# Performance work log

Hardware: AMD Instinct MI355X
Metric: run time of the kernel (lower is better)

Reference implementation:

```python
import jax, jax.numpy as jnp
import numpy as np

NH = 4       # n_heads
R = 3        # n_rounds
LN_EPS = 1e-5
NEG = -1e9   # large negative for masked attention (avoids NaN on fully-masked rows)


def _mha(q, k, v, w, b, block=None):
    # w: [4, D, D] = (Wq, Wk, Wv, Wo); b: [4, D]. batch_first MHA, no dropout (eval).
    B, Nq, Dm = q.shape
    hd = Dm // NH

    def proj(x, wi, bi):
        return (x @ wi + bi).reshape(B, -1, NH, hd).transpose(0, 2, 1, 3)  # [B,h,N,hd]

    Q = proj(q, w[0], b[0])
    K = proj(k, w[1], b[1])
    V = proj(v, w[2], b[2])
    s = jnp.einsum('bhqd,bhkd->bhqk', Q, K) * (1.0 / np.sqrt(hd))
    if block is not None:  # block[b,q,k]=True means masked out
        s = jnp.where(block[:, None, :, :], NEG, s)
    p = jax.nn.softmax(s, axis=-1)
    o = jnp.einsum('bhqk,bhkd->bhqd', p, V).transpose(0, 2, 1, 3).reshape(B, -1, Dm)
    return o @ w[3] + b[3]


def setup_inputs() -> dict:
    key = jax.random.key(0)
    ks = jax.random.split(key, 16)
    B, N, Dm = 256, 128, 256
    s = 0.02
    return {
        'H': jax.random.normal(ks[0], (B, N, Dm), jnp.float32),
        'pred_heads': jax.random.randint(ks[1], (B, N), 0, N),
        'mask': jnp.ones((B, N), jnp.float32),
        'ha_w': jax.random.normal(ks[2], (R, 4, Dm, Dm)) * s,
        'ha_b': jnp.zeros((R, 4, Dm)),
        'sa_w': jax.random.normal(ks[3], (R, 4, Dm, Dm)) * s,
        'sa_b': jnp.zeros((R, 4, Dm)),
        'ct_w': jax.random.normal(ks[4], (R, 2 * Dm, Dm)) * s,
        'ct_b': jnp.zeros((R, Dm)),
        'gate_w': jax.random.normal(ks[5], (R, 4 * Dm, Dm)) * s,
        'gate_b': jnp.zeros((R, Dm)),
        'tr_w': jax.random.normal(ks[6], (R, 4 * Dm, Dm)) * s,
        'tr_b': jnp.zeros((R, Dm)),
        'ln_g': jnp.ones((R, Dm)),
        'ln_b': jnp.zeros((R, Dm)),
        'arc_head_w': jax.random.normal(ks[7], (Dm, Dm)) * s,
        'arc_head_b': jnp.zeros((Dm,)),
        'arc_dep_w': jax.random.normal(ks[8], (Dm, Dm)) * s,
        'arc_dep_b': jnp.zeros((Dm,)),
        'bilinear': jax.random.normal(ks[9], (Dm, Dm)) * np.sqrt(2.0 / Dm).astype(np.float32),
        'bh_w': jax.random.normal(ks[10], (Dm,)) * s,
        'bh_b': jnp.zeros(()),
        'bd_w': jax.random.normal(ks[11], (Dm,)) * s,
        'bd_b': jnp.zeros(()),
    }


def reference(H, pred_heads, mask, ha_w, ha_b, sa_w, sa_b, ct_w, ct_b,
              gate_w, gate_b, tr_w, tr_b, ln_g, ln_b,
              arc_head_w, arc_head_b, arc_dep_w, arc_dep_b, bilinear,
              bh_w, bh_b, bd_w, bd_b):
    B, N, Dm = H.shape
    mb = mask > 0
    hi = jnp.clip(pred_heads, 0, N - 1)
    hi3 = jnp.broadcast_to(hi[:, :, None], (B, N, Dm))
    bidx = jnp.arange(B)[:, None]
    eye = jnp.eye(N, dtype=bool)
    # sibling mask: same predicted head, not self, both positions valid (constant across rounds)
    sib = (pred_heads[:, :, None] == pred_heads[:, None, :]) & ~eye[None] \
          & mb[:, None, :] & mb[:, :, None]
    block = ~sib

    Hr = H
    for i in range(R):
        # gather head representation, attend to it
        head_repr = jnp.take_along_axis(Hr, hi3, axis=1)
        head_msg = _mha(Hr, head_repr, head_repr, ha_w[i], ha_b[i])
        # scatter-add children onto their heads, average
        child_sum = jnp.zeros_like(Hr).at[bidx, hi].add(Hr)
        child_count = jnp.zeros((B, N), Hr.dtype).at[bidx, hi].add(mask)
        child_avg = child_sum / jnp.maximum(child_count, 1.0)[:, :, None]
        child_msg = jax.nn.gelu(
            jnp.concatenate([Hr, child_avg], -1) @ ct_w[i] + ct_b[i], approximate=False)
        # masked sibling self-attention (N <= 128 branch)
        sib_msg = _mha(Hr, Hr, Hr, sa_w[i], sa_b[i], block=block)
        # gated fuse + residual + LayerNorm
        comb = jnp.concatenate([Hr, head_msg, child_msg, sib_msg], -1)
        g = jax.nn.sigmoid(comb @ gate_w[i] + gate_b[i])
        u = jax.nn.gelu(comb @ tr_w[i] + tr_b[i], approximate=False)
        Hn = Hr + g * u
        mu = Hn.mean(-1, keepdims=True)
        var = ((Hn - mu) ** 2).mean(-1, keepdims=True)
        Hr = (Hn - mu) / jnp.sqrt(var + LN_EPS) * ln_g[i] + ln_b[i]

    h_head = Hr @ arc_head_w + arc_head_b
    h_dep = Hr @ arc_dep_w + arc_dep_b
    scores = jnp.einsum('bnd,de,bme->bnm', h_head, bilinear, h_dep)
    scores = scores + (h_head @ bh_w + bh_b)[:, None, :] + (h_dep @ bd_w + bd_b)[:, :, None]
    return Hr, scores
```

## Files before the change

kernel.cpp:

```cpp
#include <hip/hip_runtime.h>
#include <hip/hip_bf16.h>
#include <math.h>

typedef __hip_bfloat16 bf16;
typedef __attribute__((ext_vector_type(8))) short bf16x8v;
typedef __attribute__((ext_vector_type(4))) float f32x4v;

#define BD 256
#define NN 128
#define DM 256
#define NHD 4
#define HDIM 64
#define RR 3

__device__ __forceinline__ float b2f(bf16 x) { return __bfloat162float(x); }
__device__ __forceinline__ bf16 f2b(float x) { return __float2bfloat16(x); }
__device__ __forceinline__ float geluf(float x) { return 0.5f * x * (1.f + erff(x * 0.70710678118654752f)); }

#define GLOAD16(g, l) __builtin_amdgcn_global_load_lds( \
    (const __attribute__((address_space(1))) void*)(g), \
    (__attribute__((address_space(3))) void*)(l), 16, 0, 0)

__global__ __launch_bounds__(256) void cvt32to16_kernel(
    const float* __restrict__ in, bf16* __restrict__ out, int n)
{
  int i = blockIdx.x * 256 + threadIdx.x;
  int stride = gridDim.x * 256;
  for (; i < n; i += stride) out[i] = f2b(in[i]);
}

__global__ __launch_bounds__(256) void cvt16to32_kernel(
    const bf16* __restrict__ in, float* __restrict__ out, int n)
{
  int i = blockIdx.x * 256 + threadIdx.x;
  int stride = gridDim.x * 256;
  for (; i < n; i += stride) out[i] = b2f(in[i]);
}

struct TDesc { const float* src; bf16* dst; int K; int base; };
struct TTable { TDesc e[11]; };

__global__ __launch_bounds__(256) void transpose_w_kernel(TTable T, int nent)
{
  int t = blockIdx.x;
  int ei = 0;
  for (int i = 1; i < nent; i++) if (t >= T.e[i].base) ei = i;
  const float* src = T.e[ei].src;
  bf16* dst = T.e[ei].dst;
  int K = T.e[ei].K;
  int lt = t - T.e[ei].base;
  int nt = lt & 7, kt = lt >> 3;

  __shared__ float tile[32][33];
  int tx = threadIdx.x & 31, ty = threadIdx.x >> 5;
#pragma unroll
  for (int i = 0; i < 4; i++)
    tile[ty + i * 8][tx] = src[(size_t)(kt * 32 + ty + i * 8) * 256 + nt * 32 + tx];
  __syncthreads();
#pragma unroll
  for (int i = 0; i < 4; i++)
    dst[(size_t)(nt * 32 + ty + i * 8) * K + kt * 32 + tx] = f2b(tile[tx][ty + i * 8]);
}

struct ProjArgs {
  const bf16* Hc; const bf16* CA; const int* gather;
  const bf16* W[7];
  const float* bias[7];
  bf16* out[7];
};

__global__ __launch_bounds__(256) void proj_fused_kernel(ProjArgs P)
{
  const int b  = blockIdx.x & 255;
  const int nh = blockIdx.x >> 8;
  const int c0 = nh * 128;
  const int tid = threadIdx.x;
  const int w = tid >> 6;
  const int lane = tid & 63;
  const int wr = w >> 1, wc = w & 1;
  const int r16 = lane & 15;
  const int kg = lane >> 4;

  __shared__ __align__(16) char lds[81920];

  const char* Hb = (const char*)(P.Hc + (size_t)b * NN * DM);

#pragma unroll
  for (int i = 0; i < 16; i++) {
    int row = w * 32 + i * 2 + (lane >> 5);
    int src = row * 512 + (((lane & 31) * 16) ^ ((row & 7) << 4));
    GLOAD16(Hb + src, lds + w * 16384 + i * 1024);
  }

#define STAGE_W(WT, K2, KT, BUF) do { \
    _Pragma("unroll") \
    for (int i_ = 0; i_ < 2; i_++) { \
      int wrow_ = w * 32 + i_ * 16 + (lane >> 2); \
      int slot_ = (lane & 3) ^ ((wrow_ >> 1) & 3); \
      GLOAD16((const char*)(WT) + (size_t)(c0 + wrow_) * (K2) + (KT) * 64 + slot_ * 16, \
              lds + 65536 + (BUF) * 8192 + w * 2048 + i_ * 1024); \
    } } while (0)

  STAGE_W(P.W[0], 512, 0, 0);
  __syncthreads();

  int lrow[4], grow[4];
#pragma unroll
  for (int mi = 0; mi < 4; mi++) {
    lrow[mi] = wr * 64 + mi * 16 + r16;
    int g = P.gather[b * NN + lrow[mi]];
    grow[mi] = min(max(g, 0), NN - 1);
  }
  int wro[4];
#pragma unroll
  for (int ni = 0; ni < 4; ni++) {
    int ct_ = wc * 64 + ni * 16 + r16;
    wro[ni] = ct_ * 64 + ((kg ^ ((ct_ >> 1) & 3)) << 4);
  }

  const bf16* CAb = P.CA + (size_t)b * NN * DM;
  int buf = 0;
  f32x4v zero = {0.f, 0.f, 0.f, 0.f};

#pragma unroll
  for (int j = 0; j < 7; j++) {
    const bool GATH = (j == 1) || (j == 2);
    const bool TR   = (j == 2) || (j == 5);
    const bool ACT  = (j == 6);
    const int NKS = (j == 6) ? 16 : 8;
    const int K2  = (j == 6) ? 1024 : 512;
    const bf16* Wj  = P.W[j];
    const bf16* Wj1 = (j < 6) ? P.W[j + 1] : P.W[j];
    const int  K2n  = (j < 6) ? ((j + 1 == 6) ? 1024 : 512) : K2;

    f32x4v acc[4][4];
#pragma unroll
    for (int mi = 0; mi < 4; mi++)
#pragma unroll
      for (int ni = 0; ni < 4; ni++) acc[mi][ni] = zero;

    for (int kt = 0; kt < NKS; kt++) {
      if (!(j == 6 && kt + 1 == NKS)) {
        const bf16* Wn = (kt + 1 < NKS) ? Wj : Wj1;
        int nkt = (kt + 1 < NKS) ? kt + 1 : 0;
        int nK2 = (kt + 1 < NKS) ? K2 : K2n;
        STAGE_W(Wn, nK2, nkt, buf ^ 1);
      }

      bf16x8v a[4], wv[4];
      if (j == 6 && kt >= 8) {
#pragma unroll
        for (int mi = 0; mi < 4; mi++)
          a[mi] = *(const bf16x8v*)(CAb + (size_t)lrow[mi] * DM + (kt - 8) * 32 + kg * 8);
      } else {
#pragma unroll
        for (int mi = 0; mi < 4; mi++) {
          int ar = GATH ? grow[mi] : lrow[mi];
          int off = ar * 512 + (((kt * 64) + kg * 16) ^ ((ar & 7) << 4));
          a[mi] = *(const bf16x8v*)(lds + off);
        }
      }
#pragma unroll
      for (int ni = 0; ni < 4; ni++)
        wv[ni] = *(const bf16x8v*)(lds + 65536 + buf * 8192 + wro[ni]);

#pragma unroll
      for (int mi = 0; mi < 4; mi++)
#pragma unroll
        for (int ni = 0; ni < 4; ni++)
          acc[mi][ni] = __builtin_amdgcn_mfma_f32_16x16x32_bf16(a[mi], wv[ni], acc[mi][ni], 0, 0, 0);

      __syncthreads();
      buf ^= 1;
    }

    bf16* outj = P.out[j];
    const float* bj = P.bias[j];
#pragma unroll
    for (int ni = 0; ni < 4; ni++) {
      int col = c0 + wc * 64 + ni * 16 + r16;
      float bv = bj ? bj[col] : 0.f;
#pragma unroll
      for (int mi = 0; mi < 4; mi++) {
        int row0 = wr * 64 + mi * 16 + kg * 4;
        if (!TR) {
          size_t base = ((size_t)b * NN + row0) * DM + col;
#pragma unroll
          for (int r = 0; r < 4; r++) {
            float x = acc[mi][ni][r] + bv;
            if (ACT) x = geluf(x);
            outj[base + (size_t)r * DM] = f2b(x);
          }
        } else {
          size_t base = ((size_t)b * DM + col) * NN + row0;
#pragma unroll
          for (int r = 0; r < 4; r++)
            outj[base + r] = f2b(acc[mi][ni][r] + bv);
        }
      }
    }
  }
#undef STAGE_W
}

struct GJob {
  const bf16 *a0, *a1, *a2, *a3;
  const int* gather;
  const bf16* Wt;
  const float* bias;
  bf16* out;
  int K, act, transp;
};
struct GJobs8 { GJob j[8]; };

__global__ __launch_bounds__(256) void gemm_multi_kernel(GJobs8 J)
{
  const GJob jb = J.j[blockIdx.y];
  const int b  = blockIdx.x & 255;
  const int nh = blockIdx.x >> 8;
  const int tid = threadIdx.x;
  const int w = tid >> 6;
  const int lane = tid & 63;
  const int wr = w >> 1, wc = w & 1;
  const int r16 = lane & 15;
  const int kg = lane >> 4;
  const int K = jb.K;
  const int nk = K >> 5;
  const int c0 = nh * 128;

  __shared__ __align__(16) char lds[32768];

  const int srow = tid >> 2;
  const int skc  = tid & 3;
  const int sl   = skc ^ ((srow >> 1) & 3);
  int g0 = srow, g1 = srow + 64;
  if (jb.gather) {
    int t0 = jb.gather[b * NN + srow];      g0 = min(max(t0, 0), NN - 1);
    int t1 = jb.gather[b * NN + srow + 64]; g1 = min(max(t1, 0), NN - 1);
  }
  const size_t aoff0 = ((size_t)b * NN + g0) * DM + sl * 8;
  const size_t aoff1 = ((size_t)b * NN + g1) * DM + sl * 8;
  const bf16* wsrc0 = jb.Wt + (size_t)(c0 + srow) * K + sl * 8;
  const bf16* wsrc1 = jb.Wt + (size_t)(c0 + srow + 64) * K + sl * 8;
  const int wbase = w * 1024;

  f32x4v zero = {0.f, 0.f, 0.f, 0.f};
  f32x4v acc[4][4];
#pragma unroll
  for (int mi = 0; mi < 4; mi++)
#pragma unroll
    for (int ni = 0; ni < 4; ni++) acc[mi][ni] = zero;

  int a_ro[4], w_ro[4];
#pragma unroll
  for (int mi = 0; mi < 4; mi++) {
    int row = wr * 64 + mi * 16 + r16;
    a_ro[mi] = row * 64 + ((kg ^ ((row >> 1) & 3)) << 4);
  }
#pragma unroll
  for (int ni = 0; ni < 4; ni++) {
    int col = wc * 64 + ni * 16 + r16;
    w_ro[ni] = col * 64 + ((kg ^ ((col >> 1) & 3)) << 4);
  }

  {
    const bf16* Ab = jb.a0;
    GLOAD16(Ab + aoff0, lds + wbase);
    GLOAD16(Ab + aoff1, lds + 4096 + wbase);
    GLOAD16(wsrc0,      lds + 16384 + wbase);
    GLOAD16(wsrc1,      lds + 16384 + 4096 + wbase);
  }
  __syncthreads();

  int cur = 0;
  for (int kt = 0; kt < nk; kt++) {
    if (kt + 1 < nk) {
      int k0 = (kt + 1) << 5;
      int sg = k0 >> 8;
      const bf16* Ab = (sg == 0) ? jb.a0 : ((sg == 1) ? jb.a1 : ((sg == 2) ? jb.a2 : jb.a3));
      int ko = k0 & 255;
      int nb = (cur ^ 1) * 8192;
      GLOAD16(Ab + aoff0 + ko,  lds + nb + wbase);
      GLOAD16(Ab + aoff1 + ko,  lds + nb + 4096 + wbase);
      GLOAD16(wsrc0 + k0,       lds + 16384 + nb + wbase);
      GLOAD16(wsrc1 + k0,       lds + 16384 + nb + 4096 + wbase);
    }

    const char* La = lds + cur * 8192;
    const char* Lw = lds + 16384 + cur * 8192;
    bf16x8v a[4], ww[4];
#pragma unroll
    for (int mi = 0; mi < 4; mi++) a[mi] = *(const bf16x8v*)(La + a_ro[mi]);
#pragma unroll
    for (int ni = 0; ni < 4; ni++) ww[ni] = *(const bf16x8v*)(Lw + w_ro[ni]);
#pragma unroll
    for (int mi = 0; mi < 4; mi++)
#pragma unroll
      for (int ni = 0; ni < 4; ni++)
        acc[mi][ni] = __builtin_amdgcn_mfma_f32_16x16x32_bf16(a[mi], ww[ni], acc[mi][ni], 0, 0, 0);

    __syncthreads();
    cur ^= 1;
  }

#pragma unroll
  for (int ni = 0; ni < 4; ni++) {
    int col = c0 + wc * 64 + ni * 16 + r16;
    float bv = jb.bias ? jb.bias[col] : 0.f;
#pragma unroll
    for (int mi = 0; mi < 4; mi++) {
      int row0 = wr * 64 + mi * 16 + kg * 4;
      if (!jb.transp) {
        size_t base = ((size_t)b * NN + row0) * DM + col;
#pragma unroll
        for (int r = 0; r < 4; r++) {
          float x = acc[mi][ni][r] + bv;
          if (jb.act == 1) x = geluf(x);
          jb.out[base + (size_t)r * DM] = f2b(x);
        }
      } else {
        size_t base = ((size_t)b * DM + col) * NN + row0;
#pragma unroll
        for (int r = 0; r < 4; r++) {
          float x = acc[mi][ni][r] + bv;
          if (jb.act == 1) x = geluf(x);
          jb.out[base + r] = f2b(x);
        }
      }
    }
  }
}

struct AttnArgs {
  const bf16 *Qa, *Ka, *Va; bf16* Oa;
  const bf16 *Qs, *Ks, *Vs; bf16* Os;
};

__global__ __launch_bounds__(256) void attn2_kernel(
    AttnArgs A, const int* __restrict__ ph, const float* __restrict__ mask)
{
  const int b = blockIdx.y, h = blockIdx.x;
  const bool has_mask = (blockIdx.z == 1);
  const bf16* Qb = has_mask ? A.Qs : A.Qa;
  const bf16* Kb = has_mask ? A.Ks : A.Ka;
  const bf16* Vt = has_mask ? A.Vs : A.Va;
  bf16* Ob       = has_mask ? A.Os : A.Oa;

  const int w = threadIdx.x >> 6;
  const int lane = threadIdx.x & 63;
  const int r16 = lane & 15, kg = lane >> 4;
  const int q0 = w * 32;

  __shared__ bf16 P_lds[4][32 * 128];
  __shared__ int   ph_sh[NN];
  __shared__ float mk_sh[NN];

  if (has_mask && threadIdx.x < NN) {
    ph_sh[threadIdx.x] = ph[(size_t)b * NN + threadIdx.x];
    mk_sh[threadIdx.x] = mask[(size_t)b * NN + threadIdx.x];
  }
  __syncthreads();

  const bf16* Qh = Qb + (size_t)b * NN * DM + (size_t)h * HDIM;
  const bf16* Kh = Kb + (size_t)b * NN * DM + (size_t)h * HDIM;
  const bf16* Vh = Vt + ((size_t)b * DM + (size_t)h * HDIM) * NN;

  f32x4v zero = {0.f, 0.f, 0.f, 0.f};

  f32x4v accs[2][8];
#pragma unroll
  for (int mi = 0; mi < 2; mi++)
#pragma unroll
    for (int ni = 0; ni < 8; ni++) accs[mi][ni] = zero;

#pragma unroll
  for (int ks = 0; ks < 2; ks++) {
    int d = ks * 32 + kg * 8;
    bf16x8v a[2], bb[8];
#pragma unroll
    for (int mi = 0; mi < 2; mi++)
      a[mi] = *(const bf16x8v*)(Qh + (size_t)(q0 + mi * 16 + r16) * DM + d);
#pragma unroll
    for (int ni = 0; ni < 8; ni++)
      bb[ni] = *(const bf16x8v*)(Kh + (size_t)(ni * 16 + r16) * DM + d);
#pragma unroll
    for (int mi = 0; mi < 2; mi++)
#pragma unroll
      for (int ni = 0; ni < 8; ni++)
        accs[mi][ni] = __builtin_amdgcn_mfma_f32_16x16x32_bf16(a[mi], bb[ni], accs[mi][ni], 0, 0, 0);
  }

#pragma unroll
  for (int mi = 0; mi < 2; mi++) {
#pragma unroll
    for (int r = 0; r < 4; r++) {
      int wq = mi * 16 + kg * 4 + r;
      int q_e = q0 + wq;
      float v[8];
      float mx = -3.0e38f;
      int qp = 0; float qm = 1.f;
      if (has_mask) { qp = ph_sh[q_e]; qm = mk_sh[q_e]; }
#pragma unroll
      for (int ni = 0; ni < 8; ni++) {
        float s = accs[mi][ni][r] * 0.125f;
        if (has_mask) {
          int t_e = ni * 16 + r16;
          bool sib = (qp == ph_sh[t_e]) && (q_e != t_e) && (qm > 0.f) && (mk_sh[t_e] > 0.f);
          if (!sib) s = -1e9f;
        }
        v[ni] = s;
        mx = fmaxf(mx, s);
      }
#pragma unroll
      for (int o = 1; o < 16; o <<= 1) mx = fmaxf(mx, __shfl_xor(mx, o, 64));
      float sum = 0.f;
#pragma unroll
      for (int ni = 0; ni < 8; ni++) { v[ni] = __expf(v[ni] - mx); sum += v[ni]; }
#pragma unroll
      for (int o = 1; o < 16; o <<= 1) sum += __shfl_xor(sum, o, 64);
      float inv = 1.f / sum;
      int swz = (wq & 7) << 3;
#pragma unroll
      for (int ni = 0; ni < 8; ni++) {
        int t_e = ni * 16 + r16;
        P_lds[w][(wq * 128 + t_e) ^ swz] = f2b(v[ni] * inv);
      }
    }
  }
  __syncthreads();

  f32x4v acco[2][4];
#pragma unroll
  for (int mi = 0; mi < 2; mi++)
#pragma unroll
    for (int ni = 0; ni < 4; ni++) acco[mi][ni] = zero;

#pragma unroll
  for (int kt = 0; kt < 4; kt++) {
    int t = kt * 32 + kg * 8;
    bf16x8v a[2], bb[4];
#pragma unroll
    for (int mi = 0; mi < 2; mi++) {
      int wqr = mi * 16 + r16;
      int idx = (wqr * 128 + t) ^ ((wqr & 7) << 3);
      a[mi] = *(const bf16x8v*)&P_lds[w][idx];
    }
#pragma unroll
    for (int ni = 0; ni < 4; ni++)
      bb[ni] = *(const bf16x8v*)(Vh + (size_t)(ni * 16 + r16) * NN + t);
#pragma unroll
    for (int mi = 0; mi < 2; mi++)
#pragma unroll
      for (int ni = 0; ni < 4; ni++)
        acco[mi][ni] = __builtin_amdgcn_mfma_f32_16x16x32_bf16(a[mi], bb[ni], acco[mi][ni], 0, 0, 0);
  }

#pragma unroll
  for (int ni = 0; ni < 4; ni++) {
    int d = ni * 16 + r16;
#pragma unroll
    for (int mi = 0; mi < 2; mi++) {
      int qrow = q0 + mi * 16 + kg * 4;
      size_t base = ((size_t)b * NN + qrow) * DM + (size_t)h * HDIM + d;
#pragma unroll
      for (int r = 0; r < 4; r++)
        Ob[base + (size_t)r * DM] = f2b(acco[mi][ni][r]);
    }
  }
}

__global__ __launch_bounds__(256) void child_avg2_kernel(
    const bf16* __restrict__ Hr, const int* __restrict__ ph,
    const float* __restrict__ mask, bf16* __restrict__ CA)
{
  const int b = blockIdx.x;
  const int t = threadIdx.x;
  __shared__ int hi[NN];
  __shared__ float mk[NN];
  __shared__ int cnt[NN], off[NN], rnk[NN], lst[NN];
  __shared__ float cntf[NN];

  if (t < NN) {
    int g = ph[(size_t)b * NN + t];
    hi[t] = min(max(g, 0), NN - 1);
    mk[t] = mask[(size_t)b * NN + t];
  }
  __syncthreads();
  if (t < NN) {
    int c = 0, r = 0; float cf = 0.f;
    int me = hi[t];
    for (int j = 0; j < NN; j++) {
      int hj = hi[j];
      c  += (hj == t);
      cf += (hj == t) ? mk[j] : 0.f;
      r  += (j < t) && (hj == me);
    }
    cnt[t] = c; cntf[t] = cf; rnk[t] = r;
  }
  __syncthreads();
  if (t < NN) {
    int o = 0;
    for (int m = 0; m < t; m++) o += cnt[m];
    off[t] = o;
  }
  __syncthreads();
  if (t < NN) lst[off[hi[t]] + rnk[t]] = t;
  __syncthreads();

  const bf16* Hb = Hr + (size_t)b * NN * DM;
  bf16* Cb = CA + (size_t)b * NN * DM;
  const int d = t;
  for (int m = 0; m < NN; m++) {
    float s = 0.f;
    int o = off[m], c = cnt[m];
    for (int i = 0; i < c; i++)
      s += b2f(Hb[(size_t)lst[o + i] * DM + d]);
    Cb[(size_t)m * DM + d] = f2b(s / fmaxf(cntf[m], 1.f));
  }
}

__global__ __launch_bounds__(256) void ln_epi_kernel(
    const bf16* __restrict__ Hr, const bf16* __restrict__ Gp, const bf16* __restrict__ Up,
    const float* __restrict__ lg, const float* __restrict__ lb, bf16* __restrict__ Hout)
{
  const int b = blockIdx.y;
  const int m0 = blockIdx.x * 8;
  const int c = threadIdx.x;
  __shared__ float red[8];
  float lgv = lg[c], lbv = lb[c];
  int wv = c >> 6, ln = c & 63;
  for (int m = 0; m < 8; m++) {
    size_t idx = ((size_t)b * NN + m0 + m) * DM + c;
    float g = 1.f / (1.f + __expf(-b2f(Gp[idx])));
    float u = geluf(b2f(Up[idx]));
    float hn = b2f(Hr[idx]) + g * u;
    float s1 = hn, s2 = hn * hn;
#pragma unroll
    for (int o = 1; o < 64; o <<= 1) { s1 += __shfl_xor(s1, o, 64); s2 += __shfl_xor(s2, o, 64); }
    if (ln == 0) { red[wv] = s1; red[4 + wv] = s2; }
    __syncthreads();
    float sum = red[0] + red[1] + red[2] + red[3];
    float sq  = red[4] + red[5] + red[6] + red[7];
    float mu = sum * (1.f / DM);
    float var = sq * (1.f / DM) - mu * mu;
    float y = (hn - mu) * rsqrtf(var + 1e-5f) * lgv + lbv;
    Hout[idx] = f2b(y);
    __syncthreads();
  }
}

__global__ __launch_bounds__(256) void rhrd_kernel(
    const bf16* __restrict__ hh, const bf16* __restrict__ hd,
    const float* __restrict__ bhw, const float* __restrict__ bhb,
    const float* __restrict__ bdw, const float* __restrict__ bdb,
    float* __restrict__ rh, float* __restrict__ rd)
{
  int b = blockIdx.x;
  int t = threadIdx.x;
  int n = t & 127;
  bool isD = t >= 128;
  const bf16* row = (isD ? hd : hh) + ((size_t)b * NN + n) * DM;
  const float* wv = isD ? bdw : bhw;
  float s = isD ? bdb[0] : bhb[0];
  for (int k = 0; k < DM; k++) s += b2f(row[k]) * wv[k];
  (isD ? rd : rh)[(size_t)b * NN + n] = s;
}

__global__ __launch_bounds__(512) void scores_mfma_kernel(
    const bf16* __restrict__ tmp, const bf16* __restrict__ hd,
    const float* __restrict__ rh, const float* __restrict__ rd,
    float* __restrict__ out)
{
  const int b = blockIdx.x;
  const int w = threadIdx.x >> 6;
  const int lane = threadIdx.x & 63;
  const int wr = w >> 1, wc = w & 1;
  const int r16 = lane & 15;
  const int kg = lane >> 4;

  size_t qoff[2], moff[4];
#pragma unroll
  for (int mi = 0; mi < 2; mi++) qoff[mi] = ((size_t)b * NN + wr * 32 + mi * 16 + r16) * DM;
#pragma unroll
  for (int ni = 0; ni < 4; ni++) moff[ni] = ((size_t)b * NN + wc * 64 + ni * 16 + r16) * DM;

  f32x4v zero = {0.f, 0.f, 0.f, 0.f};
  f32x4v acc[2][4];
#pragma unroll
  for (int mi = 0; mi < 2; mi++)
#pragma unroll
    for (int ni = 0; ni < 4; ni++) acc[mi][ni] = zero;

  for (int k0 = 0; k0 < DM; k0 += 32) {
    int k = k0 + kg * 8;
    bf16x8v a[2], bb[4];
#pragma unroll
    for (int mi = 0; mi < 2; mi++) a[mi] = *(const bf16x8v*)(tmp + qoff[mi] + k);
#pragma unroll
    for (int ni = 0; ni < 4; ni++) bb[ni] = *(const bf16x8v*)(hd + moff[ni] + k);
#pragma unroll
    for (int mi = 0; mi < 2; mi++)
#pragma unroll
      for (int ni = 0; ni < 4; ni++)
        acc[mi][ni] = __builtin_amdgcn_mfma_f32_16x16x32_bf16(a[mi], bb[ni], acc[mi][ni], 0, 0, 0);
  }

#pragma unroll
  for (int ni = 0; ni < 4; ni++) {
    int m = wc * 64 + ni * 16 + r16;
    float rhm = rh[b * NN + m];
#pragma unroll
    for (int mi = 0; mi < 2; mi++) {
      int q0 = wr * 32 + mi * 16 + kg * 4;
#pragma unroll
      for (int r = 0; r < 4; r++)
        out[(size_t)b * NN * NN + (size_t)(q0 + r) * NN + m] =
            acc[mi][ni][r] + rhm + rd[b * NN + q0 + r];
    }
  }
}

extern "C" void kernel_launch(void* const* d_in, const int* in_sizes, int n_in,
                              void* d_out, int out_size, void* d_ws, size_t ws_size,
                              hipStream_t stream) {
  const float* H      = (const float*)d_in[0];
  const int*   ph     = (const int*)  d_in[1];
  const float* mask   = (const float*)d_in[2];
  const float* ha_w   = (const float*)d_in[3];
  const float* ha_b   = (const float*)d_in[4];
  const float* sa_w   = (const float*)d_in[5];
  const float* sa_b   = (const float*)d_in[6];
  const float* ct_w   = (const float*)d_in[7];
  const float* ct_b   = (const float*)d_in[8];
  const float* gate_w = (const float*)d_in[9];
  const float* gate_b = (const float*)d_in[10];
  const float* tr_w   = (const float*)d_in[11];
  const float* tr_b   = (const float*)d_in[12];
  const float* ln_g   = (const float*)d_in[13];
  const float* ln_b   = (const float*)d_in[14];
  const float* ahw    = (const float*)d_in[15];
  const float* ahb    = (const float*)d_in[16];
  const float* adw    = (const float*)d_in[17];
  const float* adb    = (const float*)d_in[18];
  const float* bil    = (const float*)d_in[19];
  const float* bhw    = (const float*)d_in[20];
  const float* bhb    = (const float*)d_in[21];
  const float* bdw    = (const float*)d_in[22];
  const float* bdb    = (const float*)d_in[23];

  const size_t AB = (size_t)BD * NN * DM;
  bf16* wsb  = (bf16*)d_ws;
  bf16* Hcur = wsb + 0 * AB;
  bf16* Qa   = wsb + 1 * AB;
  bf16* Ka   = wsb + 2 * AB;
  bf16* Va   = wsb + 3 * AB;
  bf16* Qs   = wsb + 4 * AB;
  bf16* Ks   = wsb + 5 * AB;
  bf16* Vs   = wsb + 6 * AB;
  bf16* mC   = wsb + 7 * AB;
  float* rh  = (float*)(wsb + 8 * AB);
  float* rd  = rh + (size_t)BD * NN;

  bf16* D0 = (bf16*)d_out;
  bf16* D1 = D0 + AB;
  bf16* D2 = D0 + 2 * AB;
  bf16* haT = D2;
  bf16* saT = D2 + 262144;
  bf16* ctT = D2 + 524288;
  bf16* gT  = D2 + 655360;
  bf16* tT  = D2 + 917504;

  cvt32to16_kernel<<<dim3(2048), 256, 0, stream>>>(H, Hcur, (int)AB);

  for (int r = 0; r < RR; r++) {
    TTable T; int base = 0;
    for (int i = 0; i < 4; i++) {
      T.e[i] = { ha_w + ((size_t)r * 4 + i) * 65536, haT + (size_t)i * 65536, 256, base };
      base += 64;
    }
    for (int i = 0; i < 4; i++) {
      T.e[4 + i] = { sa_w + ((size_t)r * 4 + i) * 65536, saT + (size_t)i * 65536, 256, base };
      base += 64;
    }
    T.e[8]  = { ct_w   + (size_t)r * 131072, ctT, 512,  base }; base += 128;
    T.e[9]  = { gate_w + (size_t)r * 262144, gT,  1024, base }; base += 256;
    T.e[10] = { tr_w   + (size_t)r * 262144, tT,  1024, base }; base += 256;
    transpose_w_kernel<<<dim3(base), 256, 0, stream>>>(T, 11);

    child_avg2_kernel<<<dim3(BD), 256, 0, stream>>>(Hcur, ph, mask, D0);

    const float* hab = ha_b + (size_t)r * 4 * DM;
    const float* sab = sa_b + (size_t)r * 4 * DM;

    {
      ProjArgs P;
      P.Hc = Hcur; P.CA = D0; P.gather = ph;
      P.W[0] = haT;          P.bias[0] = hab + 0;   P.out[0] = Qa;
      P.W[1] = haT + 65536;  P.bias[1] = hab + 256; P.out[1] = Ka;
      P.W[2] = haT + 131072; P.bias[2] = hab + 512; P.out[2] = Va;
      P.W[3] = saT;          P.bias[3] = sab + 0;   P.out[3] = Qs;
      P.W[4] = saT + 65536;  P.bias[4] = sab + 256; P.out[4] = Ks;
      P.W[5] = saT + 131072; P.bias[5] = sab + 512; P.out[5] = Vs;
      P.W[6] = ctT;          P.bias[6] = ct_b + (size_t)r * DM; P.out[6] = mC;
      proj_fused_kernel<<<dim3(512), 256, 0, stream>>>(P);
    }

    {
      AttnArgs A = { Qa, Ka, Va, D0, Qs, Ks, Vs, D1 };
      attn2_kernel<<<dim3(NHD, BD, 2), 256, 0, stream>>>(A, ph, mask);
    }

    {
      GJobs8 J = {};
      J.j[0] = { D0, D0, D0, D0, nullptr, haT + 196608, hab + 768, Ka, 256, 0, 0 };
      J.j[1] = { D1, D1, D1, D1, nullptr, saT + 196608, sab + 768, Ks, 256, 0, 0 };
      gemm_multi_kernel<<<dim3(512, 2), 256, 0, stream>>>(J);
    }

    {
      GJobs8 J = {};
      J.j[0] = { Hcur, Ka, mC, Ks, nullptr, gT, gate_b + (size_t)r * DM, Va, 1024, 0, 0 };
      J.j[1] = { Hcur, Ka, mC, Ks, nullptr, tT, tr_b   + (size_t)r * DM, Vs, 1024, 0, 0 };
      gemm_multi_kernel<<<dim3(512, 2), 256, 0, stream>>>(J);
    }

    ln_epi_kernel<<<dim3(16, BD), 256, 0, stream>>>(Hcur, Va, Vs,
        ln_g + (size_t)r * DM, ln_b + (size_t)r * DM, Hcur);
  }

  {
    TTable T;
    T.e[0] = { ahw, D2,           256, 0 };
    T.e[1] = { adw, D2 + 65536,   256, 64 };
    T.e[2] = { bil, D2 + 131072,  256, 128 };
    transpose_w_kernel<<<dim3(192), 256, 0, stream>>>(T, 3);
  }
  {
    GJobs8 J = {};
    J.j[0] = { Hcur, Hcur, Hcur, Hcur, nullptr, D2,          ahb, Qa, 256, 0, 0 };
    J.j[1] = { Hcur, Hcur, Hcur, Hcur, nullptr, D2 + 65536,  adb, Ka, 256, 0, 0 };
    gemm_multi_kernel<<<dim3(512, 2), 256, 0, stream>>>(J);
  }
  rhrd_kernel<<<dim3(BD), 256, 0, stream>>>(Qa, Ka, bhw, bhb, bdw, bdb, rh, rd);
  {
    GJobs8 J = {};
    J.j[0] = { Qa, Qa, Qa, Qa, nullptr, D2 + 131072, nullptr, Va, 256, 0, 0 };
    gemm_multi_kernel<<<dim3(512, 1), 256, 0, stream>>>(J);
  }
  scores_mfma_kernel<<<dim3(BD), 512, 0, stream>>>(Va, Ka, rh, rd, (float*)d_out + AB);

  cvt16to32_kernel<<<dim3(2048), 256, 0, stream>>>(Hcur, (float*)d_out, (int)AB);
}
```

Before: 1.027 ms.

## Stream GEMM operands directly from global memory into registers, dropping LDS weight staging

In the fused projection kernel, weight tiles are no longer staged through a double-buffered LDS region. Each lane now loads its weight fragments straight from global memory, with two register sets alternating so loads overlap the MFMAs, and the per-step barriers are removed. The generic multi-GEMM kernel is replaced by a version with no LDS that loads both operands from global memory into registers. It uses 64-column tiles, which doubles the grid. The goal is to cut LDS traffic, barrier stalls and LDS footprint so more blocks fit per CU, at the cost of less coalesced global accesses and more reliance on L2 for operand reuse.

```diff
diff --git a/kernel.cpp b/kernel.cpp
--- a/kernel.cpp
+++ b/kernel.cpp
@@ -81,7 +81,7 @@
   const int r16 = lane & 15;
   const int kg = lane >> 4;
 
-  __shared__ __align__(16) char lds[81920];
+  __shared__ __align__(16) char lds[65536];
 
   const char* Hb = (const char*)(P.Hc + (size_t)b * NN * DM);
 
@@ -91,17 +91,6 @@
     int src = row * 512 + (((lane & 31) * 16) ^ ((row & 7) << 4));
     GLOAD16(Hb + src, lds + w * 16384 + i * 1024);
   }
-
-#define STAGE_W(WT, K2, KT, BUF) do { \
-    _Pragma("unroll") \
-    for (int i_ = 0; i_ < 2; i_++) { \
-      int wrow_ = w * 32 + i_ * 16 + (lane >> 2); \
-      int slot_ = (lane & 3) ^ ((wrow_ >> 1) & 3); \
-      GLOAD16((const char*)(WT) + (size_t)(c0 + wrow_) * (K2) + (KT) * 64 + slot_ * 16, \
-              lds + 65536 + (BUF) * 8192 + w * 2048 + i_ * 1024); \
-    } } while (0)
-
-  STAGE_W(P.W[0], 512, 0, 0);
   __syncthreads();
 
   int lrow[4], grow[4];
@@ -111,15 +100,8 @@
     int g = P.gather[b * NN + lrow[mi]];
     grow[mi] = min(max(g, 0), NN - 1);
   }
-  int wro[4];
-#pragma unroll
-  for (int ni = 0; ni < 4; ni++) {
-    int ct_ = wc * 64 + ni * 16 + r16;
-    wro[ni] = ct_ * 64 + ((kg ^ ((ct_ >> 1) & 3)) << 4);
-  }
 
   const bf16* CAb = P.CA + (size_t)b * NN * DM;
-  int buf = 0;
   f32x4v zero = {0.f, 0.f, 0.f, 0.f};
 
 #pragma unroll
@@ -128,50 +110,55 @@
     const bool TR   = (j == 2) || (j == 5);
     const bool ACT  = (j == 6);
     const int NKS = (j == 6) ? 16 : 8;
-    const int K2  = (j == 6) ? 1024 : 512;
-    const bf16* Wj  = P.W[j];
-    const bf16* Wj1 = (j < 6) ? P.W[j + 1] : P.W[j];
-    const int  K2n  = (j < 6) ? ((j + 1 == 6) ? 1024 : 512) : K2;
-
-    f32x4v acc[4][4];
-#pragma unroll
-    for (int mi = 0; mi < 4; mi++)
-#pragma unroll
-      for (int ni = 0; ni < 4; ni++) acc[mi][ni] = zero;
-
-    for (int kt = 0; kt < NKS; kt++) {
-      if (!(j == 6 && kt + 1 == NKS)) {
-        const bf16* Wn = (kt + 1 < NKS) ? Wj : Wj1;
-        int nkt = (kt + 1 < NKS) ? kt + 1 : 0;
-        int nK2 = (kt + 1 < NKS) ? K2 : K2n;
-        STAGE_W(Wn, nK2, nkt, buf ^ 1);
-      }
-
-      bf16x8v a[4], wv[4];
-      if (j == 6 && kt >= 8) {
+    const int K2  = (j == 6) ? 512 : 256;
+    const bf16* __restrict__ Wj = P.W[j];
+
+    size_t wboff[4];
+#pragma unroll
+    for (int ni = 0; ni < 4; ni++)
+      wboff[ni] = (size_t)(c0 + wc * 64 + ni * 16 + r16) * K2;
+
+    auto LOADW = [&](bf16x8v* d, int ktv) {
+#pragma unroll
+      for (int ni = 0; ni < 4; ni++)
+        d[ni] = *(const bf16x8v*)(Wj + wboff[ni] + ktv * 32 + kg * 8);
+    };
+    auto LOADA = [&](bf16x8v* d, int ktv) {
+      if (j == 6 && ktv >= 8) {
 #pragma unroll
         for (int mi = 0; mi < 4; mi++)
-          a[mi] = *(const bf16x8v*)(CAb + (size_t)lrow[mi] * DM + (kt - 8) * 32 + kg * 8);
+          d[mi] = *(const bf16x8v*)(CAb + (size_t)lrow[mi] * DM + (ktv - 8) * 32 + kg * 8);
       } else {
 #pragma unroll
         for (int mi = 0; mi < 4; mi++) {
           int ar = GATH ? grow[mi] : lrow[mi];
-          int off = ar * 512 + (((kt * 64) + kg * 16) ^ ((ar & 7) << 4));
-          a[mi] = *(const bf16x8v*)(lds + off);
+          int off = ar * 512 + (((ktv * 64) + kg * 16) ^ ((ar & 7) << 4));
+          d[mi] = *(const bf16x8v*)(lds + off);
         }
       }
-#pragma unroll
-      for (int ni = 0; ni < 4; ni++)
-        wv[ni] = *(const bf16x8v*)(lds + 65536 + buf * 8192 + wro[ni]);
-
+    };
+
+    f32x4v acc[4][4];
+#pragma unroll
+    for (int mi = 0; mi < 4; mi++)
+#pragma unroll
+      for (int ni = 0; ni < 4; ni++) acc[mi][ni] = zero;
+
+    bf16x8v aA[4], wA[4], aB[4], wB[4];
+    LOADA(aA, 0); LOADW(wA, 0);
+    for (int kt = 0; kt < NKS; kt += 2) {
+      LOADA(aB, kt + 1); LOADW(wB, kt + 1);
 #pragma unroll
       for (int mi = 0; mi < 4; mi++)
 #pragma unroll
         for (int ni = 0; ni < 4; ni++)
-          acc[mi][ni] = __builtin_amdgcn_mfma_f32_16x16x32_bf16(a[mi], wv[ni], acc[mi][ni], 0, 0, 0);
-
-      __syncthreads();
-      buf ^= 1;
+          acc[mi][ni] = __builtin_amdgcn_mfma_f32_16x16x32_bf16(aA[mi], wA[ni], acc[mi][ni], 0, 0, 0);
+      if (kt + 2 < NKS) { LOADA(aA, kt + 2); LOADW(wA, kt + 2); }
+#pragma unroll
+      for (int mi = 0; mi < 4; mi++)
+#pragma unroll
+        for (int ni = 0; ni < 4; ni++)
+          acc[mi][ni] = __builtin_amdgcn_mfma_f32_16x16x32_bf16(aB[mi], wB[ni], acc[mi][ni], 0, 0, 0);
     }
 
     bf16* outj = P.out[j];
@@ -179,7 +166,7 @@
 #pragma unroll
     for (int ni = 0; ni < 4; ni++) {
       int col = c0 + wc * 64 + ni * 16 + r16;
-      float bv = bj ? bj[col] : 0.f;
+      float bv = bj[col];
 #pragma unroll
       for (int mi = 0; mi < 4; mi++) {
         int row0 = wr * 64 + mi * 16 + kg * 4;
@@ -200,7 +187,6 @@
       }
     }
   }
-#undef STAGE_W
 }
 
 struct GJob {
@@ -213,11 +199,12 @@
 };
 struct GJobs8 { GJob j[8]; };
 
-__global__ __launch_bounds__(256) void gemm_multi_kernel(GJobs8 J)
+__global__ __launch_bounds__(256) void stream_gemm_kernel(GJobs8 J)
 {
   const GJob jb = J.j[blockIdx.y];
   const int b  = blockIdx.x & 255;
-  const int nh = blockIdx.x >> 8;
+  const int cq = blockIdx.x >> 8;
+  const int c0 = cq * 64;
   const int tid = threadIdx.x;
   const int w = tid >> 6;
   const int lane = tid & 63;
@@ -226,86 +213,65 @@
   const int kg = lane >> 4;
   const int K = jb.K;
   const int nk = K >> 5;
-  const int c0 = nh * 128;
-
-  __shared__ __align__(16) char lds[32768];
-
-  const int srow = tid >> 2;
-  const int skc  = tid & 3;
-  const int sl   = skc ^ ((srow >> 1) & 3);
-  int g0 = srow, g1 = srow + 64;
-  if (jb.gather) {
-    int t0 = jb.gather[b * NN + srow];      g0 = min(max(t0, 0), NN - 1);
-    int t1 = jb.gather[b * NN + srow + 64]; g1 = min(max(t1, 0), NN - 1);
-  }
-  const size_t aoff0 = ((size_t)b * NN + g0) * DM + sl * 8;
-  const size_t aoff1 = ((size_t)b * NN + g1) * DM + sl * 8;
-  const bf16* wsrc0 = jb.Wt + (size_t)(c0 + srow) * K + sl * 8;
-  const bf16* wsrc1 = jb.Wt + (size_t)(c0 + srow + 64) * K + sl * 8;
-  const int wbase = w * 1024;
-
-  f32x4v zero = {0.f, 0.f, 0.f, 0.f};
-  f32x4v acc[4][4];
-#pragma unroll
-  for (int mi = 0; mi < 4; mi++)
-#pragma unroll
-    for (int ni = 0; ni < 4; ni++) acc[mi][ni] = zero;
-
-  int a_ro[4], w_ro[4];
+
+  size_t roff[4];
 #pragma unroll
   for (int mi = 0; mi < 4; mi++) {
     int row = wr * 64 + mi * 16 + r16;
-    a_ro[mi] = row * 64 + ((kg ^ ((row >> 1) & 3)) << 4);
-  }
-#pragma unroll
-  for (int ni = 0; ni < 4; ni++) {
-    int col = wc * 64 + ni * 16 + r16;
-    w_ro[ni] = col * 64 + ((kg ^ ((col >> 1) & 3)) << 4);
-  }
-
-  {
-    const bf16* Ab = jb.a0;
-    GLOAD16(Ab + aoff0, lds + wbase);
-    GLOAD16(Ab + aoff1, lds + 4096 + wbase);
-    GLOAD16(wsrc0,      lds + 16384 + wbase);
-    GLOAD16(wsrc1,      lds + 16384 + 4096 + wbase);
-  }
-  __syncthreads();
-
-  int cur = 0;
-  for (int kt = 0; kt < nk; kt++) {
-    if (kt + 1 < nk) {
-      int k0 = (kt + 1) << 5;
-      int sg = k0 >> 8;
-      const bf16* Ab = (sg == 0) ? jb.a0 : ((sg == 1) ? jb.a1 : ((sg == 2) ? jb.a2 : jb.a3));
-      int ko = k0 & 255;
-      int nb = (cur ^ 1) * 8192;
-      GLOAD16(Ab + aoff0 + ko,  lds + nb + wbase);
-      GLOAD16(Ab + aoff1 + ko,  lds + nb + 4096 + wbase);
-      GLOAD16(wsrc0 + k0,       lds + 16384 + nb + wbase);
-      GLOAD16(wsrc1 + k0,       lds + 16384 + nb + 4096 + wbase);
-    }
-
-    const char* La = lds + cur * 8192;
-    const char* Lw = lds + 16384 + cur * 8192;
-    bf16x8v a[4], ww[4];
-#pragma unroll
-    for (int mi = 0; mi < 4; mi++) a[mi] = *(const bf16x8v*)(La + a_ro[mi]);
-#pragma unroll
-    for (int ni = 0; ni < 4; ni++) ww[ni] = *(const bf16x8v*)(Lw + w_ro[ni]);
+    if (jb.gather) { int g = jb.gather[b * NN + row]; row = min(max(g, 0), NN - 1); }
+    roff[mi] = ((size_t)b * NN + row) * DM;
+  }
+  size_t woff[2];
+#pragma unroll
+  for (int ni = 0; ni < 2; ni++)
+    woff[ni] = (size_t)(c0 + wc * 32 + ni * 16 + r16) * K;
+
+  const bf16* __restrict__ A0 = jb.a0;
+  const bf16* __restrict__ A1 = jb.a1;
+  const bf16* __restrict__ A2 = jb.a2;
+  const bf16* __restrict__ A3 = jb.a3;
+  const bf16* __restrict__ Wt = jb.Wt;
+
+  auto LA = [&](bf16x8v* d, int ktv) {
+    int k = ktv * 32 + kg * 8;
+    const bf16* __restrict__ Ab = (k < 256) ? A0 : ((k < 512) ? A1 : ((k < 768) ? A2 : A3));
 #pragma unroll
     for (int mi = 0; mi < 4; mi++)
-#pragma unroll
-      for (int ni = 0; ni < 4; ni++)
-        acc[mi][ni] = __builtin_amdgcn_mfma_f32_16x16x32_bf16(a[mi], ww[ni], acc[mi][ni], 0, 0, 0);
-
-    __syncthreads();
-    cur ^= 1;
-  }
-
-#pragma unroll
-  for (int ni = 0; ni < 4; ni++) {
-    int col = c0 + wc * 64 + ni * 16 + r16;
+      d[mi] = *(const bf16x8v*)(Ab + roff[mi] + (k & 255));
+  };
+  auto LW = [&](bf16x8v* d, int ktv) {
+#pragma unroll
+    for (int ni = 0; ni < 2; ni++)
+      d[ni] = *(const bf16x8v*)(Wt + woff[ni] + ktv * 32 + kg * 8);
+  };
+
+  f32x4v zero = {0.f, 0.f, 0.f, 0.f};
+  f32x4v acc[4][2];
+#pragma unroll
+  for (int mi = 0; mi < 4; mi++)
+#pragma unroll
+    for (int ni = 0; ni < 2; ni++) acc[mi][ni] = zero;
+
+  bf16x8v aA[4], wA[2], aB[4], wB[2];
+  LA(aA, 0); LW(wA, 0);
+  for (int kt = 0; kt < nk; kt += 2) {
+    LA(aB, kt + 1); LW(wB, kt + 1);
+#pragma unroll
+    for (int mi = 0; mi < 4; mi++)
+#pragma unroll
+      for (int ni = 0; ni < 2; ni++)
+        acc[mi][ni] = __builtin_amdgcn_mfma_f32_16x16x32_bf16(aA[mi], wA[ni], acc[mi][ni], 0, 0, 0);
+    if (kt + 2 < nk) { LA(aA, kt + 2); LW(wA, kt + 2); }
+#pragma unroll
+    for (int mi = 0; mi < 4; mi++)
+#pragma unroll
+      for (int ni = 0; ni < 2; ni++)
+        acc[mi][ni] = __builtin_amdgcn_mfma_f32_16x16x32_bf16(aB[mi], wB[ni], acc[mi][ni], 0, 0, 0);
+  }
+
+#pragma unroll
+  for (int ni = 0; ni < 2; ni++) {
+    int col = c0 + wc * 32 + ni * 16 + r16;
     float bv = jb.bias ? jb.bias[col] : 0.f;
 #pragma unroll
     for (int mi = 0; mi < 4; mi++) {
@@ -714,14 +680,14 @@
       GJobs8 J = {};
       J.j[0] = { D0, D0, D0, D0, nullptr, haT + 196608, hab + 768, Ka, 256, 0, 0 };
       J.j[1] = { D1, D1, D1, D1, nullptr, saT + 196608, sab + 768, Ks, 256, 0, 0 };
-      gemm_multi_kernel<<<dim3(512, 2), 256, 0, stream>>>(J);
+      stream_gemm_kernel<<<dim3(1024, 2), 256, 0, stream>>>(J);
     }
 
     {
       GJobs8 J = {};
       J.j[0] = { Hcur, Ka, mC, Ks, nullptr, gT, gate_b + (size_t)r * DM, Va, 1024, 0, 0 };
       J.j[1] = { Hcur, Ka, mC, Ks, nullptr, tT, tr_b   + (size_t)r * DM, Vs, 1024, 0, 0 };
-      gemm_multi_kernel<<<dim3(512, 2), 256, 0, stream>>>(J);
+      stream_gemm_kernel<<<dim3(1024, 2), 256, 0, stream>>>(J);
     }
 
     ln_epi_kernel<<<dim3(16, BD), 256, 0, stream>>>(Hcur, Va, Vs,
@@ -739,13 +705,13 @@
     GJobs8 J = {};
     J.j[0] = { Hcur, Hcur, Hcur, Hcur, nullptr, D2,          ahb, Qa, 256, 0, 0 };
     J.j[1] = { Hcur, Hcur, Hcur, Hcur, nullptr, D2 + 65536,  adb, Ka, 256, 0, 0 };
-    gemm_multi_kernel<<<dim3(512, 2), 256, 0, stream>>>(J);
+    stream_gemm_kernel<<<dim3(1024, 2), 256, 0, stream>>>(J);
   }
   rhrd_kernel<<<dim3(BD), 256, 0, stream>>>(Qa, Ka, bhw, bhb, bdw, bdb, rh, rd);
   {
     GJobs8 J = {};
     J.j[0] = { Qa, Qa, Qa, Qa, nullptr, D2 + 131072, nullptr, Va, 256, 0, 0 };
-    gemm_multi_kernel<<<dim3(512, 1), 256, 0, stream>>>(J);
+    stream_gemm_kernel<<<dim3(1024, 1), 256, 0, stream>>>(J);
   }
   scores_mfma_kernel<<<dim3(BD), 512, 0, stream>>>(Va, Ka, rh, rd, (float*)d_out + AB);
 
```

New measurement: 1.830 ms. 1.78x slower.

## Fold attention output projections into gate/transform weights and arc-head into bilinear

Applied to the files above, without the earlier changes.

Precomputes Wo·Wgate and Wo·Wtr products (and biases) so the per-round output-projection GEMMs for both attention branches disappear, feeding attention outputs directly into the 1024-wide gate/transform GEMM. Similarly folds arc_head_w into the bilinear matrix and the head bias vector, removing one final GEMM and the separate bilinear GEMM. All weight transposes are hoisted before the round loop. This trades activation GEMMs for small weight-only GEMMs done with a naive fp32 kernel, and the products are rounded to bf16, which can change numerics slightly.

```diff
diff --git a/kernel.cpp b/kernel.cpp
--- a/kernel.cpp
+++ b/kernel.cpp
@@ -38,7 +38,7 @@
 }
 
 struct TDesc { const float* src; bf16* dst; int K; int base; };
-struct TTable { TDesc e[11]; };
+struct TTable { TDesc e[12]; };
 
 __global__ __launch_bounds__(256) void transpose_w_kernel(TTable T, int nent)
 {
@@ -60,6 +60,64 @@
 #pragma unroll
   for (int i = 0; i < 4; i++)
     dst[(size_t)(nt * 32 + ty + i * 8) * K + kt * 32 + tx] = f2b(tile[tx][ty + i * 8]);
+}
+
+struct FJob { const float* A; const float* B; bf16* outT; int koff; int kst; };
+struct FJobs { FJob j[13]; };
+
+__global__ __launch_bounds__(256) void wfuse_kernel(FJobs F)
+{
+  const FJob jb = F.j[blockIdx.y];
+  const int k0 = blockIdx.x * 16;
+  const int col = threadIdx.x;
+  float acc[16];
+#pragma unroll
+  for (int i = 0; i < 16; i++) acc[i] = 0.f;
+  for (int m = 0; m < 256; m++) {
+    float bv = jb.B[(size_t)m * 256 + col];
+#pragma unroll
+    for (int i = 0; i < 16; i++)
+      acc[i] += jb.A[(size_t)(k0 + i) * 256 + m] * bv;
+  }
+#pragma unroll
+  for (int i = 0; i < 16; i++)
+    jb.outT[(size_t)col * jb.kst + jb.koff + k0 + i] = f2b(acc[i]);
+}
+
+__global__ __launch_bounds__(256) void bfuse_kernel(
+    const float* gate_w, const float* tr_w, const float* gate_b, const float* tr_b,
+    const float* ha_b, const float* sa_b,
+    const float* ahw, const float* ahb, const float* bil,
+    const float* bhw, const float* bhb,
+    float* fgb, float* ftb, float* fab_bias, float* vha, float* cha)
+{
+  int blk = blockIdx.x, col = threadIdx.x;
+  if (blk < 6) {
+    int r = blk >> 1; bool isT = blk & 1;
+    const float* W  = (isT ? tr_w : gate_w) + (size_t)r * 262144;
+    const float* b0 = (isT ? tr_b : gate_b) + (size_t)r * 256;
+    const float* boh = ha_b + (size_t)r * 1024 + 768;
+    const float* bos = sa_b + (size_t)r * 1024 + 768;
+    float acc = b0[col];
+    for (int m = 0; m < 256; m++) {
+      acc += boh[m] * W[(size_t)(256 + m) * 256 + col];
+      acc += bos[m] * W[(size_t)(768 + m) * 256 + col];
+    }
+    ((isT ? ftb : fgb) + (size_t)r * 256)[col] = acc;
+  } else {
+    float a1 = 0.f, a2 = 0.f;
+    for (int m = 0; m < 256; m++) {
+      a1 += ahb[m] * bil[(size_t)m * 256 + col];
+      a2 += ahw[(size_t)col * 256 + m] * bhw[m];
+    }
+    fab_bias[col] = a1;
+    vha[col] = a2;
+    if (col == 0) {
+      float c = bhb[0];
+      for (int m = 0; m < 256; m++) c += ahb[m] * bhw[m];
+      cha[0] = c;
+    }
+  }
 }
 
 struct ProjArgs {
@@ -549,9 +607,9 @@
   }
 }
 
-__global__ __launch_bounds__(256) void rhrd_kernel(
-    const bf16* __restrict__ hh, const bf16* __restrict__ hd,
-    const float* __restrict__ bhw, const float* __restrict__ bhb,
+__global__ __launch_bounds__(256) void rhrd2_kernel(
+    const bf16* __restrict__ Hc, const bf16* __restrict__ hd,
+    const float* __restrict__ vha, const float* __restrict__ cha,
     const float* __restrict__ bdw, const float* __restrict__ bdb,
     float* __restrict__ rh, float* __restrict__ rd)
 {
@@ -559,11 +617,17 @@
   int t = threadIdx.x;
   int n = t & 127;
   bool isD = t >= 128;
-  const bf16* row = (isD ? hd : hh) + ((size_t)b * NN + n) * DM;
-  const float* wv = isD ? bdw : bhw;
-  float s = isD ? bdb[0] : bhb[0];
-  for (int k = 0; k < DM; k++) s += b2f(row[k]) * wv[k];
-  (isD ? rd : rh)[(size_t)b * NN + n] = s;
+  if (!isD) {
+    const bf16* row = Hc + ((size_t)b * NN + n) * DM;
+    float s = cha[0];
+    for (int k = 0; k < DM; k++) s += b2f(row[k]) * vha[k];
+    rh[(size_t)b * NN + n] = s;
+  } else {
+    const bf16* row = hd + ((size_t)b * NN + n) * DM;
+    float s = bdb[0];
+    for (int k = 0; k < DM; k++) s += b2f(row[k]) * bdw[k];
+    rd[(size_t)b * NN + n] = s;
+  }
 }
 
 __global__ __launch_bounds__(512) void scores_mfma_kernel(
@@ -660,37 +724,77 @@
   bf16* mC   = wsb + 7 * AB;
   float* rh  = (float*)(wsb + 8 * AB);
   float* rd  = rh + (size_t)BD * NN;
+  float* fgb = rd + (size_t)BD * NN;
+  float* ftb = fgb + 768;
+  float* fab_bias = ftb + 768;
+  float* vha = fab_bias + 256;
+  float* cha = vha + 256;
 
   bf16* D0 = (bf16*)d_out;
   bf16* D1 = D0 + AB;
   bf16* D2 = D0 + 2 * AB;
-  bf16* haT = D2;
-  bf16* saT = D2 + 262144;
-  bf16* ctT = D2 + 524288;
-  bf16* gT  = D2 + 655360;
-  bf16* tT  = D2 + 917504;
+  const size_t RS = 1179648;
+  bf16* adT  = D2 + 3 * RS;
+  bf16* fabT = adT + 65536;
 
   cvt32to16_kernel<<<dim3(2048), 256, 0, stream>>>(H, Hcur, (int)AB);
 
   for (int r = 0; r < RR; r++) {
+    bf16* base_r = D2 + (size_t)r * RS;
+    bf16* haT = base_r;
+    bf16* saT = base_r + 262144;
+    bf16* ctT = base_r + 524288;
+    bf16* gT  = base_r + 655360;
+    bf16* tT  = base_r + 917504;
     TTable T; int base = 0;
-    for (int i = 0; i < 4; i++) {
+    for (int i = 0; i < 3; i++) {
       T.e[i] = { ha_w + ((size_t)r * 4 + i) * 65536, haT + (size_t)i * 65536, 256, base };
       base += 64;
     }
-    for (int i = 0; i < 4; i++) {
-      T.e[4 + i] = { sa_w + ((size_t)r * 4 + i) * 65536, saT + (size_t)i * 65536, 256, base };
+    for (int i = 0; i < 3; i++) {
+      T.e[3 + i] = { sa_w + ((size_t)r * 4 + i) * 65536, saT + (size_t)i * 65536, 256, base };
       base += 64;
     }
-    T.e[8]  = { ct_w   + (size_t)r * 131072, ctT, 512,  base }; base += 128;
-    T.e[9]  = { gate_w + (size_t)r * 262144, gT,  1024, base }; base += 256;
-    T.e[10] = { tr_w   + (size_t)r * 262144, tT,  1024, base }; base += 256;
-    transpose_w_kernel<<<dim3(base), 256, 0, stream>>>(T, 11);
-
-    child_avg2_kernel<<<dim3(BD), 256, 0, stream>>>(Hcur, ph, mask, D0);
-
+    T.e[6] = { ct_w + (size_t)r * 131072, ctT, 512, base };                    base += 128;
+    T.e[7] = { gate_w + (size_t)r * 262144,             gT,        1024, base }; base += 64;
+    T.e[8] = { gate_w + (size_t)r * 262144 + 512 * 256, gT + 512,  1024, base }; base += 64;
+    T.e[9] = { tr_w   + (size_t)r * 262144,             tT,        1024, base }; base += 64;
+    T.e[10]= { tr_w   + (size_t)r * 262144 + 512 * 256, tT + 512,  1024, base }; base += 64;
+    int nent = 11;
+    if (r == 0) { T.e[11] = { adw, adT, 256, base }; base += 64; nent = 12; }
+    transpose_w_kernel<<<dim3(base), 256, 0, stream>>>(T, nent);
+  }
+  {
+    FJobs F;
+    for (int r = 0; r < RR; r++) {
+      bf16* gT = D2 + (size_t)r * RS + 655360;
+      bf16* tT = D2 + (size_t)r * RS + 917504;
+      const float* WoH = ha_w + ((size_t)r * 4 + 3) * 65536;
+      const float* WoS = sa_w + ((size_t)r * 4 + 3) * 65536;
+      const float* gw = gate_w + (size_t)r * 262144;
+      const float* tw = tr_w   + (size_t)r * 262144;
+      F.j[r * 4 + 0] = { WoH, gw + 256 * 256, gT, 256, 1024 };
+      F.j[r * 4 + 1] = { WoS, gw + 768 * 256, gT, 768, 1024 };
+      F.j[r * 4 + 2] = { WoH, tw + 256 * 256, tT, 256, 1024 };
+      F.j[r * 4 + 3] = { WoS, tw + 768 * 256, tT, 768, 1024 };
+    }
+    F.j[12] = { ahw, bil, fabT, 0, 256 };
+    wfuse_kernel<<<dim3(16, 13), 256, 0, stream>>>(F);
+  }
+  bfuse_kernel<<<dim3(7), 256, 0, stream>>>(gate_w, tr_w, gate_b, tr_b,
+      ha_b, sa_b, ahw, ahb, bil, bhw, bhb, fgb, ftb, fab_bias, vha, cha);
+
+  for (int r = 0; r < RR; r++) {
+    bf16* base_r = D2 + (size_t)r * RS;
+    bf16* haT = base_r;
+    bf16* saT = base_r + 262144;
+    bf16* ctT = base_r + 524288;
+    bf16* gT  = base_r + 655360;
+    bf16* tT  = base_r + 917504;
     const float* hab = ha_b + (size_t)r * 4 * DM;
     const float* sab = sa_b + (size_t)r * 4 * DM;
+
+    child_avg2_kernel<<<dim3(BD), 256, 0, stream>>>(Hcur, ph, mask, D0);
 
     {
       ProjArgs P;
@@ -712,15 +816,8 @@
 
     {
       GJobs8 J = {};
-      J.j[0] = { D0, D0, D0, D0, nullptr, haT + 196608, hab + 768, Ka, 256, 0, 0 };
-      J.j[1] = { D1, D1, D1, D1, nullptr, saT + 196608, sab + 768, Ks, 256, 0, 0 };
-      gemm_multi_kernel<<<dim3(512, 2), 256, 0, stream>>>(J);
-    }
-
-    {
-      GJobs8 J = {};
-      J.j[0] = { Hcur, Ka, mC, Ks, nullptr, gT, gate_b + (size_t)r * DM, Va, 1024, 0, 0 };
-      J.j[1] = { Hcur, Ka, mC, Ks, nullptr, tT, tr_b   + (size_t)r * DM, Vs, 1024, 0, 0 };
+      J.j[0] = { Hcur, D0, mC, D1, nullptr, gT, fgb + (size_t)r * 256, Va, 1024, 0, 0 };
+      J.j[1] = { Hcur, D0, mC, D1, nullptr, tT, ftb + (size_t)r * 256, Vs, 1024, 0, 0 };
       gemm_multi_kernel<<<dim3(512, 2), 256, 0, stream>>>(J);
     }
 
@@ -729,24 +826,12 @@
   }
 
   {
-    TTable T;
-    T.e[0] = { ahw, D2,           256, 0 };
-    T.e[1] = { adw, D2 + 65536,   256, 64 };
-    T.e[2] = { bil, D2 + 131072,  256, 128 };
-    transpose_w_kernel<<<dim3(192), 256, 0, stream>>>(T, 3);
-  }
-  {
     GJobs8 J = {};
-    J.j[0] = { Hcur, Hcur, Hcur, Hcur, nullptr, D2,          ahb, Qa, 256, 0, 0 };
-    J.j[1] = { Hcur, Hcur, Hcur, Hcur, nullptr, D2 + 65536,  adb, Ka, 256, 0, 0 };
+    J.j[0] = { Hcur, Hcur, Hcur, Hcur, nullptr, adT,  adb,      Ka, 256, 0, 0 };
+    J.j[1] = { Hcur, Hcur, Hcur, Hcur, nullptr, fabT, fab_bias, Va, 256, 0, 0 };
     gemm_multi_kernel<<<dim3(512, 2), 256, 0, stream>>>(J);
   }
-  rhrd_kernel<<<dim3(BD), 256, 0, stream>>>(Qa, Ka, bhw, bhb, bdw, bdb, rh, rd);
-  {
-    GJobs8 J = {};
-    J.j[0] = { Qa, Qa, Qa, Qa, nullptr, D2 + 131072, nullptr, Va, 256, 0, 0 };
-    gemm_multi_kernel<<<dim3(512, 1), 256, 0, stream>>>(J);
-  }
+  rhrd2_kernel<<<dim3(BD), 256, 0, stream>>>(Hcur, Ka, vha, cha, bdw, bdb, rh, rd);
   scores_mfma_kernel<<<dim3(BD), 512, 0, stream>>>(Va, Ka, rh, rd, (float*)d_out + AB);
 
   cvt16to32_kernel<<<dim3(2048), 256, 0, stream>>>(Hcur, (float*)d_out, (int)AB);
```

Result: no change. 1.012 ms (-1.4%).
